# Kernel optimization log

Hardware: AMD Instinct MI355X
Metric: run time of the kernel (lower is better)

## Reference

```python
import jax, jax.numpy as jnp
import numpy as np

LN_EPS = 1e-5

def _conv2d(x, w, b, pad):
    # x: [B,C,H,W], w: [O,I,kh,kw] -> [B,O,H,W]
    y = jax.lax.conv_general_dilated(
        x, w, window_strides=(1, 1), padding=[(pad, pad), (pad, pad)],
        dimension_numbers=('NCHW', 'OIHW', 'NCHW'))
    return y + b[None, :, None, None]

def setup_inputs() -> dict:
    key = jax.random.key(0)
    ks = jax.random.split(key, 12)
    B, C, H, W = 4, 256, 64, 64
    D = 64  # inner_projection
    s_in = 1.0 / np.sqrt(C)
    s_d1 = 1.0 / np.sqrt(D)
    s_d3 = 1.0 / np.sqrt(D * 9)
    return {
        'x':     jax.random.normal(ks[0], (B, C, H, W), jnp.float32),
        'w_in':  jax.random.normal(ks[1], (D, C, 1, 1), jnp.float32) * s_in,
        'b_in':  jnp.zeros((D,), jnp.float32),
        'wq':    jax.random.normal(ks[2], (D, D, 3, 3), jnp.float32) * s_d3,
        'bq':    jnp.zeros((D,), jnp.float32),
        'wk':    jax.random.normal(ks[3], (D, D, 3, 3), jnp.float32) * s_d3,
        'bk':    jnp.zeros((D,), jnp.float32),
        'wv':    jax.random.normal(ks[4], (D, D, 3, 3), jnp.float32) * s_d3,
        'bv':    jnp.zeros((D,), jnp.float32),
        'w_out': jax.random.normal(ks[5], (C, D, 1, 1), jnp.float32) * s_d1,
        'b_out': jnp.zeros((C,), jnp.float32),
        'gamma': jax.random.normal(ks[6], (1,), jnp.float32) * 0.1,
        'ln_w':  jnp.ones((C,), jnp.float32),
        'ln_b':  jnp.zeros((C,), jnp.float32),
    }

def _attention(q, k, v):
    # full-pixel attention, NO 1/sqrt(d) scale (matches source)
    B, C, H, W = v.shape
    N = H * W
    qf = q.reshape(B, -1, N)   # [B,d,N]
    kf = k.reshape(B, -1, N)
    vf = v.reshape(B, -1, N)
    energy = jnp.einsum('bci,bcj->bij', qf, kf)      # [B,N,N] = Q^T K
    attn = jax.nn.softmax(energy, axis=-1)
    out = jnp.einsum('bcj,bij->bci', vf, attn)        # V @ attn^T
    return out.reshape(B, C, H, W)

def _layernorm2d(x, w, b):
    # normalize over channel dim per pixel (LayerNorm2d)
    mu = jnp.mean(x, axis=1, keepdims=True)
    var = jnp.var(x, axis=1, keepdims=True)
    xn = (x - mu) * jax.lax.rsqrt(var + LN_EPS)
    return xn * w[None, :, None, None] + b[None, :, None, None]

def reference(x, w_in, b_in, wq, bq, wk, bk, wv, bv, w_out, b_out, gamma, ln_w, ln_b):
    att = _conv2d(x, w_in, b_in, 0)          # inner projection [B,D,H,W]
    q = _conv2d(att, wq, bq, 1)
    k = _conv2d(att, wk, bk, 1)
    v = _conv2d(att, wv, bv, 1)
    att = _attention(q, k, v)
    att = _conv2d(att, w_out, b_out, 0)       # outer projection [B,C,H,W]
    return _layernorm2d(gamma * x + att, ln_w, ln_b)
```

## Files before the change

kernel.cpp:

```cpp
#include <hip/hip_runtime.h>
#include <hip/hip_bf16.h>

#define BB 4
#define CC 256
#define DD 64
#define HH 64
#define WW 64
#define NN 4096
#define NSPLIT 4
#define VST 68
#define SM_SHIFT2 92.332482616893664f
#define LOG2E 1.4426950408889634f

typedef __hip_bfloat16 bf16;
typedef __attribute__((ext_vector_type(8))) short bf16x8;
typedef __attribute__((ext_vector_type(4))) float f32x4;
typedef __attribute__((ext_vector_type(4))) short s16x4;

#define MFMA16(a, b, c) __builtin_amdgcn_mfma_f32_16x16x32_bf16(a, b, c, 0, 0, 0)

#if __has_builtin(__builtin_amdgcn_mfma_f32_16x16x16bf16_1k)
static __device__ __forceinline__ f32x4 MFMA16K(s16x4 a, s16x4 b, f32x4 c) {
  return __builtin_amdgcn_mfma_f32_16x16x16bf16_1k(a, b, c, 0, 0, 0);
}
#else
static __device__ __forceinline__ f32x4 MFMA16K(s16x4 a, s16x4 b, f32x4 c) {
  f32x4 d;
  asm("v_mfma_f32_16x16x16_bf16 %0, %1, %2, %3"
      : "=&v"(d) : "v"(a), "v"(b), "v"(c));
  return d;
}
#endif

#if __has_builtin(__builtin_amdgcn_exp2f)
#define EXP2F(x) __builtin_amdgcn_exp2f(x)
#else
#define EXP2F(x) exp2f(x)
#endif

static __device__ __forceinline__ float ldin(const void* p, size_t i, bool isb) {
  return isb ? __bfloat162float(((const bf16*)p)[i]) : ((const float*)p)[i];
}
static __device__ __forceinline__ void stout(void* p, size_t i, float v, bool isb) {
  if (isb) ((bf16*)p)[i] = __float2bfloat16(v);
  else     ((float*)p)[i] = v;
}
static __device__ __forceinline__ unsigned pack2(bf16 a, bf16 b) {
  unsigned short ua = *reinterpret_cast<unsigned short*>(&a);
  unsigned short ub = *reinterpret_cast<unsigned short*>(&b);
  return (unsigned)ua | ((unsigned)ub << 16);
}
static __device__ __forceinline__ bool probe_bf16(const unsigned* lnw) {
  return lnw[0] == 0x3F803F80u;
}

__global__ __launch_bounds__(256) void k_wt(
    const void* __restrict__ wq, const void* __restrict__ wk,
    const void* __restrict__ wv, const void* __restrict__ w_in,
    const void* __restrict__ w_out,
    bf16* __restrict__ Wth, bf16* __restrict__ Wtl,
    bf16* __restrict__ Win_h, bf16* __restrict__ Win_l,
    bf16* __restrict__ Wo_h, bf16* __restrict__ Wo_l,
    const unsigned* __restrict__ lnw) {
  const bool isb = probe_bf16(lnw);
  int u = blockIdx.x * 256 + threadIdx.x;
  if (u < 110592) {
    int c3 = u / 36864, rem = u % 36864;
    int tap = rem / 4096, r2 = rem % 4096;
    int oc = r2 >> 6, ic = r2 & 63;
    const void* w = (c3 == 0) ? wq : ((c3 == 1) ? wk : wv);
    float v = ldin(w, (size_t)oc * 576 + ic * 9 + tap, isb);
    bf16 h = __float2bfloat16(v);
    Wth[u] = h;
    Wtl[u] = __float2bfloat16(v - __bfloat162float(h));
  } else if (u < 126976) {
    int v2 = u - 110592;
    float v = ldin(w_in, v2, isb);
    bf16 h = __float2bfloat16(v);
    Win_h[v2] = h;
    Win_l[v2] = __float2bfloat16(v - __bfloat162float(h));
  } else {
    int v2 = u - 126976;
    float v = ldin(w_out, v2, isb);
    bf16 h = __float2bfloat16(v);
    Wo_h[v2] = h;
    Wo_l[v2] = __float2bfloat16(v - __bfloat162float(h));
  }
}

__global__ __launch_bounds__(256) void k_conv_in(
    const void* __restrict__ x,
    const bf16* __restrict__ Win_h, const bf16* __restrict__ Win_l,
    const void* __restrict__ bias, bf16* __restrict__ att_h,
    bf16* __restrict__ att_l, const unsigned* __restrict__ lnw) {
  __shared__ __align__(16) short Xh[32 * 64];
  __shared__ __align__(16) short Xl[32 * 64];
  const bool isb = probe_bf16(lnw);
  const int b = blockIdx.y, n0 = blockIdx.x * 32;
  const int t = threadIdx.x;
  const int w = t >> 6, lane = t & 63, quad = lane >> 4, l16 = lane & 15;
  const int l7 = l16 & 7;
  const size_t xoff = (size_t)b * CC * NN;
  const int sdd = t >> 3, sn4 = (t & 7) * 4;
  f32x4 acc[2];
  #pragma unroll
  for (int nt = 0; nt < 2; ++nt)
    #pragma unroll
    for (int r = 0; r < 4; ++r)
      acc[nt][r] = ldin(bias, w * 16 + quad * 4 + r, isb);
  for (int c0 = 0; c0 < CC; c0 += 64) {
    __syncthreads();
    {
      float a0[4], a1[4];
      size_t i0a = xoff + (size_t)(c0 + 2 * sdd) * NN + n0 + sn4;
      if (!isb) {
        const float* xp = (const float*)x;
        float4 va = *(const float4*)&xp[i0a];
        float4 vb = *(const float4*)&xp[i0a + NN];
        a0[0] = va.x; a0[1] = va.y; a0[2] = va.z; a0[3] = va.w;
        a1[0] = vb.x; a1[1] = vb.y; a1[2] = vb.z; a1[3] = vb.w;
      } else {
        #pragma unroll
        for (int j = 0; j < 4; ++j) {
          a0[j] = ldin(x, i0a + j, true);
          a1[j] = ldin(x, i0a + NN + j, true);
        }
      }
      #pragma unroll
      for (int j = 0; j < 4; ++j) {
        int n = sn4 + j;
        bf16 h0 = __float2bfloat16(a0[j]), h1 = __float2bfloat16(a1[j]);
        bf16 l0 = __float2bfloat16(a0[j] - __bfloat162float(h0));
        bf16 l1 = __float2bfloat16(a1[j] - __bfloat162float(h1));
        int cs = ((sdd >> 2) ^ (n & 7)) * 8 + ((2 * sdd) & 7);
        *(unsigned*)&Xh[n * 64 + cs] = pack2(h0, h1);
        *(unsigned*)&Xl[n * 64 + cs] = pack2(l0, l1);
      }
    }
    __syncthreads();
    #pragma unroll
    for (int kc = 0; kc < 2; ++kc) {
      size_t woff = (size_t)(w * 16 + l16) * 256 + c0 + kc * 32 + quad * 8;
      bf16x8 wh = *(const bf16x8*)(Win_h + woff);
      bf16x8 wl = *(const bf16x8*)(Win_l + woff);
      const int xo = ((kc * 4 + quad) ^ l7) * 8;
      #pragma unroll
      for (int nt = 0; nt < 2; ++nt) {
        int rn = nt * 16 + l16;
        bf16x8 xh = *(const bf16x8*)&Xh[rn * 64 + xo];
        bf16x8 xl = *(const bf16x8*)&Xl[rn * 64 + xo];
        acc[nt] = MFMA16(wh, xh, acc[nt]);
        acc[nt] = MFMA16(wh, xl, acc[nt]);
        acc[nt] = MFMA16(wl, xh, acc[nt]);
      }
    }
  }
  #pragma unroll
  for (int nt = 0; nt < 2; ++nt) {
    size_t off = ((size_t)b * NN + n0 + nt * 16 + l16) * DD + w * 16 + quad * 4;
    bf16 h[4], l[4];
    #pragma unroll
    for (int r = 0; r < 4; ++r) {
      float v = acc[nt][r];
      h[r] = __float2bfloat16(v);
      l[r] = __float2bfloat16(v - __bfloat162float(h[r]));
    }
    *(uint2*)&att_h[off] = make_uint2(pack2(h[0], h[1]), pack2(h[2], h[3]));
    *(uint2*)&att_l[off] = make_uint2(pack2(l[0], l[1]), pack2(l[2], l[3]));
  }
}

__global__ __launch_bounds__(256) void k_conv3(
    const bf16* __restrict__ att_h, const bf16* __restrict__ att_l,
    const bf16* __restrict__ Wth, const bf16* __restrict__ Wtl,
    const void* __restrict__ bq, const void* __restrict__ bk,
    const void* __restrict__ bv,
    bf16* __restrict__ qth, bf16* __restrict__ qtl,
    bf16* __restrict__ kth, bf16* __restrict__ ktl,
    bf16* __restrict__ vt, const unsigned* __restrict__ lnw) {
  __shared__ __align__(16) short Ah[3 * 66 * 64];
  __shared__ __align__(16) short Al[3 * 66 * 64];
  float* o_s = reinterpret_cast<float*>(Ah);
  const bool isb = probe_bf16(lnw);
  const int y = blockIdx.x, b = blockIdx.y, c3 = blockIdx.z;
  const int t = threadIdx.x;
  const int w = t >> 6, lane = t & 63, quad = lane >> 4, l16 = lane & 15;
  const uint4 z4 = make_uint4(0, 0, 0, 0);
  #pragma unroll
  for (int r = 0; r < 3; ++r) {
    int yp = y + r - 1;
    bool ok = (unsigned)yp < 64u;
    const uint4* sh = (const uint4*)(att_h + ((size_t)b * NN + (size_t)yp * 64) * DD);
    const uint4* sl = (const uint4*)(att_l + ((size_t)b * NN + (size_t)yp * 64) * DD);
    #pragma unroll
    for (int ii = 0; ii < 2; ++ii) {
      int u = t + ii * 256;
      int xx = u >> 3, ch = u & 7;
      int rr = r * 66 + xx + 1;
      uint4 vh = ok ? sh[u] : z4;
      uint4 vl = ok ? sl[u] : z4;
      int cs = (ch ^ (rr & 7)) * 8;
      *(uint4*)&Ah[rr * 64 + cs] = vh;
      *(uint4*)&Al[rr * 64 + cs] = vl;
    }
    if (t < 16) {
      int rr = r * 66 + ((t & 1) ? 65 : 0);
      int cs = (t >> 1) * 8;
      *(uint4*)&Ah[rr * 64 + cs] = z4;
      *(uint4*)&Al[rr * 64 + cs] = z4;
    }
  }
  __syncthreads();
  const void* bp = (c3 == 0) ? bq : ((c3 == 1) ? bk : bv);
  const bf16* wth = Wth + (size_t)c3 * 9 * 4096;
  const bf16* wtl = Wtl + (size_t)c3 * 9 * 4096;
  f32x4 acc[4];
  #pragma unroll
  for (int nt = 0; nt < 4; ++nt)
    #pragma unroll
    for (int r = 0; r < 4; ++r)
      acc[nt][r] = ldin(bp, w * 16 + quad * 4 + r, isb);
  #pragma unroll
  for (int tap = 0; tap < 9; ++tap) {
    const int dy = tap / 3, dx = tap % 3;
    const int woff = tap * 4096 + (w * 16 + l16) * 64 + quad * 8;
    bf16x8 wh0 = *(const bf16x8*)(wth + woff);
    bf16x8 wh1 = *(const bf16x8*)(wth + woff + 32);
    bf16x8 wl0 = *(const bf16x8*)(wtl + woff);
    bf16x8 wl1 = *(const bf16x8*)(wtl + woff + 32);
    #pragma unroll
    for (int nt = 0; nt < 4; ++nt) {
      int rr = dy * 66 + nt * 16 + l16 + dx;
      int chA = (quad ^ (rr & 7)) * 8;
      int chB = ((quad + 4) ^ (rr & 7)) * 8;
      bf16x8 ah0 = *(const bf16x8*)&Ah[rr * 64 + chA];
      bf16x8 ah1 = *(const bf16x8*)&Ah[rr * 64 + chB];
      bf16x8 al0 = *(const bf16x8*)&Al[rr * 64 + chA];
      bf16x8 al1 = *(const bf16x8*)&Al[rr * 64 + chB];
      acc[nt] = MFMA16(wh0, ah0, acc[nt]);
      acc[nt] = MFMA16(wh1, ah1, acc[nt]);
      acc[nt] = MFMA16(wh0, al0, acc[nt]);
      acc[nt] = MFMA16(wh1, al1, acc[nt]);
      acc[nt] = MFMA16(wl0, ah0, acc[nt]);
      acc[nt] = MFMA16(wl1, ah1, acc[nt]);
    }
  }
  if (c3 < 2) {
    bf16* dh = (c3 == 0) ? qth : kth;
    bf16* dl = (c3 == 0) ? qtl : ktl;
    const float qsc = (c3 == 0) ? LOG2E : 1.0f;
    const size_t rowb = (size_t)b * NN + (size_t)y * 64;
    #pragma unroll
    for (int nt = 0; nt < 4; ++nt) {
      size_t off = (rowb + nt * 16 + l16) * DD + w * 16 + quad * 4;
      bf16 h[4], l[4];
      #pragma unroll
      for (int r = 0; r < 4; ++r) {
        float v = acc[nt][r] * qsc;
        h[r] = __float2bfloat16(v);
        l[r] = __float2bfloat16(v - __bfloat162float(h[r]));
      }
      *(uint2*)&dh[off] = make_uint2(pack2(h[0], h[1]), pack2(h[2], h[3]));
      *(uint2*)&dl[off] = make_uint2(pack2(l[0], l[1]), pack2(l[2], l[3]));
    }
  } else {
    __syncthreads();
    #pragma unroll
    for (int nt = 0; nt < 4; ++nt)
      #pragma unroll
      for (int r = 0; r < 4; ++r)
        o_s[(nt * 16 + l16) * 65 + w * 16 + quad * 4 + r] = acc[nt][r];
    __syncthreads();
    #pragma unroll
    for (int i = 0; i < 8; ++i) {
      int u = t + i * 256;
      int c = u >> 5, np = (u & 31) * 2;
      float v0 = o_s[np * 65 + c], v1 = o_s[(np + 1) * 65 + c];
      *(unsigned*)&vt[((size_t)b * DD + c) * NN + (size_t)y * 64 + np] =
          pack2(__float2bfloat16(v0), __float2bfloat16(v1));
    }
  }
}

__global__ __launch_bounds__(256) void k_attn(
    const bf16* __restrict__ qth, const bf16* __restrict__ qtl,
    const bf16* __restrict__ kth, const bf16* __restrict__ ktl,
    const bf16* __restrict__ vt, float* __restrict__ po,
    float* __restrict__ pl) {
  __shared__ __align__(16) short Kh[2][64 * 64];
  __shared__ __align__(16) short Kl[2][64 * 64];
  __shared__ __align__(16) short Vs[3][64 * VST];
  const int b = blockIdx.y, i0 = blockIdx.x * 128, sp = blockIdx.z;
  const int jt0 = sp * (64 / NSPLIT), jt1 = jt0 + (64 / NSPLIT);
  const int t = threadIdx.x;
  const int w = t >> 6, lane = t & 63, quad = lane >> 4, l16 = lane & 15;
  const int l7 = l16 & 7;
  const int xA = (quad ^ l7) * 8;
  const int xB = ((quad + 4) ^ l7) * 8;
  const int sr = t >> 2, m4 = t & 3, sg = m4 * 16;
  const int sc0 = ((2 * m4) ^ (sr & 7)) * 8;
  const int sc1 = ((2 * m4 + 1) ^ (sr & 7)) * 8;
  bf16x8 qf_h0[2], qf_h1[2], qf_l0[2], qf_l1[2];
  #pragma unroll
  for (int is = 0; is < 2; ++is) {
    size_t qoff = ((size_t)b * NN + i0 + is * 64 + w * 16 + l16) * DD + quad * 8;
    qf_h0[is] = *(const bf16x8*)(qth + qoff);
    qf_h1[is] = *(const bf16x8*)(qth + qoff + 32);
    qf_l0[is] = *(const bf16x8*)(qtl + qoff);
    qf_l1[is] = *(const bf16x8*)(qtl + qoff + 32);
  }
  const bf16* khg = kth + ((size_t)b * NN + jt0 * 64 + sr) * DD + sg;
  const bf16* klg = ktl + ((size_t)b * NN + jt0 * 64 + sr) * DD + sg;
  const bf16* vg  = vt  + ((size_t)b * DD + sr) * NN + jt0 * 64 + sg;
  uint4 kh0, kh1, kl0, kl1, vx0, vx1;
  const int s0 = jt0 % 3;
  kh0 = ((const uint4*)khg)[0]; kh1 = ((const uint4*)khg)[1];
  kl0 = ((const uint4*)klg)[0]; kl1 = ((const uint4*)klg)[1];
  vx0 = ((const uint4*)vg)[0];  vx1 = ((const uint4*)vg)[1];
  khg += 64 * DD; klg += 64 * DD; vg += 64;
  *(uint4*)&Kh[0][sr * 64 + sc0] = kh0;    *(uint4*)&Kh[0][sr * 64 + sc1] = kh1;
  *(uint4*)&Kl[0][sr * 64 + sc0] = kl0;    *(uint4*)&Kl[0][sr * 64 + sc1] = kl1;
  *(uint4*)&Vs[s0][sr * VST + sc0] = vx0;  *(uint4*)&Vs[s0][sr * VST + sc1] = vx1;
  kh0 = ((const uint4*)khg)[0]; kh1 = ((const uint4*)khg)[1];
  kl0 = ((const uint4*)klg)[0]; kl1 = ((const uint4*)klg)[1];
  vx0 = ((const uint4*)vg)[0];  vx1 = ((const uint4*)vg)[1];
  khg += 64 * DD; klg += 64 * DD; vg += 64;
  __syncthreads();
  s16x4 onesf;
  onesf[0] = onesf[1] = onesf[2] = onesf[3] = (short)0x3F80;
  f32x4 lacc[2] = {};
  f32x4 oacc[4][2] = {};
  s16x4 pfP[2][4];
  int vw = (s0 + 1 == 3) ? 0 : s0 + 1;
  int vr = s0;
  {
    const short* khp = Kh[0];
    const short* klp = Kl[0];
    __builtin_amdgcn_s_setprio(1);
    #pragma unroll
    for (int mt = 0; mt < 4; ++mt) {
      int r0 = (mt * 16 + l16) * 64;
      bf16x8 kf_h0 = *(const bf16x8*)&khp[r0 + xA];
      bf16x8 kf_h1 = *(const bf16x8*)&khp[r0 + xB];
      bf16x8 kf_l0 = *(const bf16x8*)&klp[r0 + xA];
      bf16x8 kf_l1 = *(const bf16x8*)&klp[r0 + xB];
      f32x4 c0 = {0.f, 0.f, 0.f, 0.f}, c1 = {0.f, 0.f, 0.f, 0.f};
      c0 = MFMA16(kf_h0, qf_h0[0], c0);  c0 = MFMA16(kf_h1, qf_h1[0], c0);
      c0 = MFMA16(kf_h0, qf_l0[0], c0);  c0 = MFMA16(kf_h1, qf_l1[0], c0);
      c0 = MFMA16(kf_l0, qf_h0[0], c0);  c0 = MFMA16(kf_l1, qf_h1[0], c0);
      c1 = MFMA16(kf_h0, qf_h0[1], c1);  c1 = MFMA16(kf_h1, qf_h1[1], c1);
      c1 = MFMA16(kf_h0, qf_l0[1], c1);  c1 = MFMA16(kf_h1, qf_l1[1], c1);
      c1 = MFMA16(kf_l0, qf_h0[1], c1);  c1 = MFMA16(kf_l1, qf_h1[1], c1);
      #pragma unroll
      for (int r = 0; r < 4; ++r) {
        float e0 = EXP2F(c0[r] - SM_SHIFT2);
        float e1 = EXP2F(c1[r] - SM_SHIFT2);
        bf16 p0 = __float2bfloat16(e0), p1 = __float2bfloat16(e1);
        pfP[0][mt][r] = *reinterpret_cast<short*>(&p0);
        pfP[1][mt][r] = *reinterpret_cast<short*>(&p1);
      }
    }
    __builtin_amdgcn_s_setprio(0);
    *(uint4*)&Kh[1][sr * 64 + sc0] = kh0;    *(uint4*)&Kh[1][sr * 64 + sc1] = kh1;
    *(uint4*)&Kl[1][sr * 64 + sc0] = kl0;    *(uint4*)&Kl[1][sr * 64 + sc1] = kl1;
    *(uint4*)&Vs[vw][sr * VST + sc0] = vx0;  *(uint4*)&Vs[vw][sr * VST + sc1] = vx1;
    vw = (vw + 1 == 3) ? 0 : vw + 1;
    kh0 = ((const uint4*)khg)[0]; kh1 = ((const uint4*)khg)[1];
    kl0 = ((const uint4*)klg)[0]; kl1 = ((const uint4*)klg)[1];
    vx0 = ((const uint4*)vg)[0];  vx1 = ((const uint4*)vg)[1];
    khg += 64 * DD; klg += 64 * DD; vg += 64;
    __syncthreads();
  }
  for (int jt = jt0 + 1; jt < jt1; ++jt) {
    const short* khp = Kh[jt & 1];
    const short* klp = Kl[jt & 1];
    const short* vpp = Vs[vr];
    s16x4 pfC[2][4];
    __builtin_amdgcn_s_setprio(1);
    #pragma unroll
    for (int mt = 0; mt < 4; ++mt) {
      int r0 = (mt * 16 + l16) * 64;
      bf16x8 kf_h0 = *(const bf16x8*)&khp[r0 + xA];
      bf16x8 kf_h1 = *(const bf16x8*)&khp[r0 + xB];
      bf16x8 kf_l0 = *(const bf16x8*)&klp[r0 + xA];
      bf16x8 kf_l1 = *(const bf16x8*)&klp[r0 + xB];
      f32x4 c0 = {0.f, 0.f, 0.f, 0.f}, c1 = {0.f, 0.f, 0.f, 0.f};
      c0 = MFMA16(kf_h0, qf_h0[0], c0);  c0 = MFMA16(kf_h1, qf_h1[0], c0);
      c0 = MFMA16(kf_h0, qf_l0[0], c0);  c0 = MFMA16(kf_h1, qf_l1[0], c0);
      c0 = MFMA16(kf_l0, qf_h0[0], c0);  c0 = MFMA16(kf_l1, qf_h1[0], c0);
      c1 = MFMA16(kf_h0, qf_h0[1], c1);  c1 = MFMA16(kf_h1, qf_h1[1], c1);
      c1 = MFMA16(kf_h0, qf_l0[1], c1);  c1 = MFMA16(kf_h1, qf_l1[1], c1);
      c1 = MFMA16(kf_l0, qf_h0[1], c1);  c1 = MFMA16(kf_l1, qf_h1[1], c1);
      {
        int rv = (mt * 16 + l16) * VST;
        #pragma unroll
        for (int kt = 0; kt < 4; ++kt) {
          s16x4 vf = *(const s16x4*)
              &vpp[rv + ((kt * 2 + (quad >> 1)) ^ l7) * 8 + (quad & 1) * 4];
          oacc[mt][0] = MFMA16K(vf, pfP[0][kt], oacc[mt][0]);
          oacc[mt][1] = MFMA16K(vf, pfP[1][kt], oacc[mt][1]);
        }
        lacc[0] = MFMA16K(onesf, pfP[0][mt], lacc[0]);
        lacc[1] = MFMA16K(onesf, pfP[1][mt], lacc[1]);
      }
      #pragma unroll
      for (int r = 0; r < 4; ++r) {
        float e0 = EXP2F(c0[r] - SM_SHIFT2);
        float e1 = EXP2F(c1[r] - SM_SHIFT2);
        bf16 p0 = __float2bfloat16(e0), p1 = __float2bfloat16(e1);
        pfC[0][mt][r] = *reinterpret_cast<short*>(&p0);
        pfC[1][mt][r] = *reinterpret_cast<short*>(&p1);
      }
    }
    __builtin_amdgcn_s_setprio(0);
    if (jt + 1 < jt1) {
      short* khn = Kh[(jt + 1) & 1];
      short* kln = Kl[(jt + 1) & 1];
      short* vsn = Vs[vw];
      *(uint4*)&khn[sr * 64 + sc0] = kh0;  *(uint4*)&khn[sr * 64 + sc1] = kh1;
      *(uint4*)&kln[sr * 64 + sc0] = kl0;  *(uint4*)&kln[sr * 64 + sc1] = kl1;
      *(uint4*)&vsn[sr * VST + sc0] = vx0; *(uint4*)&vsn[sr * VST + sc1] = vx1;
    }
    vw = (vw + 1 == 3) ? 0 : vw + 1;
    vr = (vr + 1 == 3) ? 0 : vr + 1;
    if (jt + 2 < jt1) {
      kh0 = ((const uint4*)khg)[0]; kh1 = ((const uint4*)khg)[1];
      kl0 = ((const uint4*)klg)[0]; kl1 = ((const uint4*)klg)[1];
      vx0 = ((const uint4*)vg)[0];  vx1 = ((const uint4*)vg)[1];
      khg += 64 * DD; klg += 64 * DD; vg += 64;
    }
    __syncthreads();
    #pragma unroll
    for (int is = 0; is < 2; ++is)
      #pragma unroll
      for (int m2 = 0; m2 < 4; ++m2) pfP[is][m2] = pfC[is][m2];
  }
  {
    const short* vpp = Vs[vr];
    __builtin_amdgcn_s_setprio(1);
    #pragma unroll
    for (int mt = 0; mt < 4; ++mt) {
      int rv = (mt * 16 + l16) * VST;
      #pragma unroll
      for (int kt = 0; kt < 4; ++kt) {
        s16x4 vf = *(const s16x4*)
            &vpp[rv + ((kt * 2 + (quad >> 1)) ^ l7) * 8 + (quad & 1) * 4];
        oacc[mt][0] = MFMA16K(vf, pfP[0][kt], oacc[mt][0]);
        oacc[mt][1] = MFMA16K(vf, pfP[1][kt], oacc[mt][1]);
      }
      lacc[0] = MFMA16K(onesf, pfP[0][mt], lacc[0]);
      lacc[1] = MFMA16K(onesf, pfP[1][mt], lacc[1]);
    }
    __builtin_amdgcn_s_setprio(0);
  }
  const size_t SEGC = (size_t)BB * DD * NN;
  #pragma unroll
  for (int is = 0; is < 2; ++is) {
    const int ig = i0 + is * 64 + w * 16 + l16;
    #pragma unroll
    for (int mt = 0; mt < 4; ++mt)
      #pragma unroll
      for (int r = 0; r < 4; ++r) {
        int c = mt * 16 + quad * 4 + r;
        po[(size_t)sp * SEGC + ((size_t)b * DD + c) * NN + ig] = oacc[mt][is][r];
      }
    if (quad == 0) pl[((size_t)sp * BB + b) * NN + ig] = lacc[is][0];
  }
}

__global__ __launch_bounds__(256) void k_out_ln(
    const float* __restrict__ po, const float* __restrict__ pl,
    const void* __restrict__ x,
    const bf16* __restrict__ Wo_h, const bf16* __restrict__ Wo_l,
    const void* __restrict__ bias, const void* __restrict__ gamma,
    const void* __restrict__ lw, const void* __restrict__ lb,
    void* __restrict__ out, const unsigned* __restrict__ lnw) {
  __shared__ __align__(16) short Ahs[32 * 64];
  __shared__ __align__(16) short Als[32 * 64];
  __shared__ __align__(16) float Obuf[256 * 36];
  __shared__ float inv_s[32];
  __shared__ float red1[32 * 4], red2[32 * 4];
  __shared__ float mu_s[32], rs_s[32];
  __shared__ float lw_s[256], lb_s[256];
  const bool isb = probe_bf16(lnw);
  const int b = blockIdx.y, n0 = blockIdx.x * 32;
  const int t = threadIdx.x;
  const int w = t >> 6, lane = t & 63, quad = lane >> 4, l16 = lane & 15;
  const int l7 = l16 & 7;
  const size_t SEGC = (size_t)BB * DD * NN;
  if (t < 32) {
    int i = n0 + t;
    float lsum = 0.f;
    #pragma unroll
    for (int s = 0; s < NSPLIT; ++s) lsum += pl[((size_t)s * BB + b) * NN + i];
    inv_s[t] = 1.f / lsum;
  }
  lw_s[t] = ldin(lw, t, isb);
  lb_s[t] = ldin(lb, t, isb);
  const float g = ldin(gamma, 0, isb);
  __syncthreads();
  {
    const int dd = t >> 3, n4 = (t & 7) * 4;
    size_t base = ((size_t)b * DD + 2 * dd) * NN + n0 + n4;
    float v0[4] = {0.f, 0.f, 0.f, 0.f}, v1[4] = {0.f, 0.f, 0.f, 0.f};
    #pragma unroll
    for (int s = 0; s < NSPLIT; ++s) {
      float4 pa = *(const float4*)&po[(size_t)s * SEGC + base];
      float4 pb = *(const float4*)&po[(size_t)s * SEGC + base + NN];
      v0[0] += pa.x; v0[1] += pa.y; v0[2] += pa.z; v0[3] += pa.w;
      v1[0] += pb.x; v1[1] += pb.y; v1[2] += pb.z; v1[3] += pb.w;
    }
    #pragma unroll
    for (int j = 0; j < 4; ++j) {
      int n = n4 + j;
      float inv = inv_s[n];
      float a0 = v0[j] * inv, a1 = v1[j] * inv;
      bf16 h0 = __float2bfloat16(a0), h1 = __float2bfloat16(a1);
      bf16 l0 = __float2bfloat16(a0 - __bfloat162float(h0));
      bf16 l1 = __float2bfloat16(a1 - __bfloat162float(h1));
      int cs = ((dd >> 2) ^ (n & 7)) * 8 + ((2 * dd) & 7);
      *(unsigned*)&Ahs[n * 64 + cs] = pack2(h0, h1);
      *(unsigned*)&Als[n * 64 + cs] = pack2(l0, l1);
    }
  }
  f32x4 acc[4][2];
  #pragma unroll
  for (int oct = 0; oct < 4; ++oct)
    #pragma unroll
    for (int r = 0; r < 4; ++r) {
      float bo = ldin(bias, w * 64 + oct * 16 + quad * 4 + r, isb);
      #pragma unroll
      for (int nt = 0; nt < 2; ++nt) acc[oct][nt][r] = bo;
    }
  __syncthreads();
  #pragma unroll
  for (int oct = 0; oct < 4; ++oct) {
    const int base = w * 64 + oct * 16;
    #pragma unroll
    for (int kc = 0; kc < 2; ++kc) {
      size_t woff = (size_t)(base + l16) * 64 + kc * 32 + quad * 8;
      bf16x8 wh = *(const bf16x8*)(Wo_h + woff);
      bf16x8 wl = *(const bf16x8*)(Wo_l + woff);
      const int xo = ((kc * 4 + quad) ^ l7) * 8;
      #pragma unroll
      for (int nt = 0; nt < 2; ++nt) {
        int rn = nt * 16 + l16;
        bf16x8 ah = *(const bf16x8*)&Ahs[rn * 64 + xo];
        bf16x8 al = *(const bf16x8*)&Als[rn * 64 + xo];
        acc[oct][nt] = MFMA16(wh, ah, acc[oct][nt]);
        acc[oct][nt] = MFMA16(wh, al, acc[oct][nt]);
        acc[oct][nt] = MFMA16(wl, ah, acc[oct][nt]);
      }
    }
  }
  #pragma unroll
  for (int nt = 0; nt < 2; ++nt) {
    int nn = nt * 16 + l16;
    float s1 = 0.f, s2 = 0.f;
    #pragma unroll
    for (int oct = 0; oct < 4; ++oct)
      #pragma unroll
      for (int r = 0; r < 4; ++r) {
        int oc = w * 64 + oct * 16 + quad * 4 + r;
        float xv = ldin(x, ((size_t)b * CC + oc) * NN + n0 + nn, isb);
        float y = acc[oct][nt][r] + g * xv;
        acc[oct][nt][r] = y;
        s1 += y; s2 += y * y;
      }
    s1 += __shfl_xor(s1, 16, 64); s1 += __shfl_xor(s1, 32, 64);
    s2 += __shfl_xor(s2, 16, 64); s2 += __shfl_xor(s2, 32, 64);
    if (quad == 0) { red1[nn * 4 + w] = s1; red2[nn * 4 + w] = s2; }
  }
  __syncthreads();
  if (t < 32) {
    float sm = red1[t * 4] + red1[t * 4 + 1] + red1[t * 4 + 2] + red1[t * 4 + 3];
    float sq = red2[t * 4] + red2[t * 4 + 1] + red2[t * 4 + 2] + red2[t * 4 + 3];
    float mu = sm * (1.f / 256.f);
    float var = sq * (1.f / 256.f) - mu * mu;
    mu_s[t] = mu;
    rs_s[t] = rsqrtf(var + 1e-5f);
  }
  __syncthreads();
  if (!isb) {
    #pragma unroll
    for (int nt = 0; nt < 2; ++nt) {
      int nn = nt * 16 + l16;
      float mu = mu_s[nn], rs = rs_s[nn];
      #pragma unroll
      for (int oct = 0; oct < 4; ++oct)
        #pragma unroll
        for (int r = 0; r < 4; ++r) {
          int oc = w * 64 + oct * 16 + quad * 4 + r;
          Obuf[oc * 36 + nn] = (acc[oct][nt][r] - mu) * rs * lw_s[oc] + lb_s[oc];
        }
    }
    __syncthreads();
    const int oc8 = t >> 3, pxq = (t & 7) * 4;
    float* op = (float*)out + (size_t)b * CC * NN + n0 + pxq;
    #pragma unroll
    for (int p2 = 0; p2 < 8; ++p2) {
      int oc = p2 * 32 + oc8;
      float4 v = *(const float4*)&Obuf[oc * 36 + pxq];
      *(float4*)&op[(size_t)oc * NN] = v;
    }
  } else {
    #pragma unroll
    for (int nt = 0; nt < 2; ++nt) {
      int nn = nt * 16 + l16;
      float mu = mu_s[nn], rs = rs_s[nn];
      #pragma unroll
      for (int oct = 0; oct < 4; ++oct)
        #pragma unroll
        for (int r = 0; r < 4; ++r) {
          int oc = w * 64 + oct * 16 + quad * 4 + r;
          float o = (acc[oct][nt][r] - mu) * rs * lw_s[oc] + lb_s[oc];
          stout(out, ((size_t)b * CC + oc) * NN + n0 + nn, o, isb);
        }
    }
  }
}

extern "C" void kernel_launch(void* const* d_in, const int* in_sizes, int n_in,
                              void* d_out, int out_size, void* d_ws, size_t ws_size,
                              hipStream_t stream) {
  const void* x     = d_in[0];
  const void* w_in  = d_in[1];
  const void* b_in  = d_in[2];
  const void* wq    = d_in[3];
  const void* bq    = d_in[4];
  const void* wk    = d_in[5];
  const void* bk    = d_in[6];
  const void* wv    = d_in[7];
  const void* bv    = d_in[8];
  const void* w_out = d_in[9];
  const void* b_out = d_in[10];
  const void* gamma = d_in[11];
  const void* ln_w  = d_in[12];
  const void* ln_b  = d_in[13];

  const size_t SEG = (size_t)BB * DD * NN;
  char*  p     = (char*)d_ws;
  bf16*  att_h = (bf16*)p;  p += SEG * 2;
  bf16*  att_l = (bf16*)p;  p += SEG * 2;
  bf16*  qth   = (bf16*)p;  p += SEG * 2;
  bf16*  qtl   = (bf16*)p;  p += SEG * 2;
  bf16*  kth   = (bf16*)p;  p += SEG * 2;
  bf16*  ktl   = (bf16*)p;  p += SEG * 2;
  bf16*  vt    = (bf16*)p;  p += SEG * 2;
  float* po    = (float*)p; p += (size_t)NSPLIT * SEG * 4;
  float* pl    = (float*)p; p += (size_t)NSPLIT * BB * NN * 4;
  bf16*  Wth   = (bf16*)p;  p += 110592 * 2;
  bf16*  Wtl   = (bf16*)p;  p += 110592 * 2;
  bf16*  Win_h = (bf16*)p;  p += 16384 * 2;
  bf16*  Win_l = (bf16*)p;  p += 16384 * 2;
  bf16*  Wo_h  = (bf16*)p;  p += 16384 * 2;
  bf16*  Wo_l  = (bf16*)p;  p += 16384 * 2;
  const unsigned* lnw = (const unsigned*)ln_w;

  k_wt<<<560, 256, 0, stream>>>(wq, wk, wv, w_in, w_out, Wth, Wtl,
                                Win_h, Win_l, Wo_h, Wo_l, lnw);
  k_conv_in<<<dim3(NN / 32, BB), 256, 0, stream>>>(x, Win_h, Win_l, b_in,
                                                   att_h, att_l, lnw);
  k_conv3<<<dim3(64, BB, 3), 256, 0, stream>>>(att_h, att_l, Wth, Wtl,
                                               bq, bk, bv,
                                               qth, qtl, kth, ktl, vt, lnw);
  k_attn<<<dim3(NN / 128, BB, NSPLIT), 256, 0, stream>>>(qth, qtl, kth, ktl, vt,
                                                         po, pl);
  k_out_ln<<<dim3(NN / 32, BB), 256, 0, stream>>>(po, pl, x, Wo_h, Wo_l,
                                                  b_out, gamma, ln_w, ln_b,
                                                  d_out, lnw);
}
```

Measured before the change: 172.8 us.

## Unroll attention pipeline by two with ping-pong registers and remap block IDs

The attention main loop becomes a macro body unrolled in pairs, with pfA and pfB swapping roles. This removes the per-iteration register copy of probabilities and the modulo buffer index arithmetic, and precomputes V swizzle offsets. Block indices are also remapped so that the eight consecutive launch IDs spread across splits, batches and query tiles, which changes cache and XCD locality. The loop trip count is hardcoded to the NSPLIT=4 tile count (16 iterations), so changing NSPLIT would break it.

```diff
diff --git a/kernel.cpp b/kernel.cpp
--- a/kernel.cpp
+++ b/kernel.cpp
@@ -282,6 +282,59 @@
   }
 }
 
+#define ATTN_BODY(PFIN, PFOUT, KRDH, KRDL, KSTH, KSTL, DOSTAGE, DOPREF)       \
+  {                                                                           \
+    __builtin_amdgcn_s_setprio(1);                                            \
+    _Pragma("unroll")                                                         \
+    for (int mt = 0; mt < 4; ++mt) {                                          \
+      int r0 = (mt * 16 + l16) * 64;                                          \
+      bf16x8 kf_h0 = *(const bf16x8*)&KRDH[r0 + xA];                          \
+      bf16x8 kf_h1 = *(const bf16x8*)&KRDH[r0 + xB];                          \
+      bf16x8 kf_l0 = *(const bf16x8*)&KRDL[r0 + xA];                          \
+      bf16x8 kf_l1 = *(const bf16x8*)&KRDL[r0 + xB];                          \
+      f32x4 c0 = {0.f, 0.f, 0.f, 0.f}, c1 = {0.f, 0.f, 0.f, 0.f};             \
+      c0 = MFMA16(kf_h0, qf_h0[0], c0);  c0 = MFMA16(kf_h1, qf_h1[0], c0);    \
+      c0 = MFMA16(kf_h0, qf_l0[0], c0);  c0 = MFMA16(kf_h1, qf_l1[0], c0);    \
+      c0 = MFMA16(kf_l0, qf_h0[0], c0);  c0 = MFMA16(kf_l1, qf_h1[0], c0);    \
+      c1 = MFMA16(kf_h0, qf_h0[1], c1);  c1 = MFMA16(kf_h1, qf_h1[1], c1);    \
+      c1 = MFMA16(kf_h0, qf_l0[1], c1);  c1 = MFMA16(kf_h1, qf_l1[1], c1);    \
+      c1 = MFMA16(kf_l0, qf_h0[1], c1);  c1 = MFMA16(kf_l1, qf_h1[1], c1);    \
+      {                                                                       \
+        int rv = (mt * 16 + l16) * VST;                                       \
+        _Pragma("unroll")                                                     \
+        for (int kt = 0; kt < 4; ++kt) {                                      \
+          s16x4 vf = *(const s16x4*)&vR[rv + vofs[kt]];                       \
+          oacc[mt][0] = MFMA16K(vf, PFIN[0][kt], oacc[mt][0]);                \
+          oacc[mt][1] = MFMA16K(vf, PFIN[1][kt], oacc[mt][1]);                \
+        }                                                                     \
+        lacc[0] = MFMA16K(onesf, PFIN[0][mt], lacc[0]);                       \
+        lacc[1] = MFMA16K(onesf, PFIN[1][mt], lacc[1]);                       \
+      }                                                                       \
+      _Pragma("unroll")                                                       \
+      for (int r = 0; r < 4; ++r) {                                           \
+        float e0 = EXP2F(c0[r] - SM_SHIFT2);                                  \
+        float e1 = EXP2F(c1[r] - SM_SHIFT2);                                  \
+        bf16 p0 = __float2bfloat16(e0), p1 = __float2bfloat16(e1);            \
+        PFOUT[0][mt][r] = *reinterpret_cast<short*>(&p0);                     \
+        PFOUT[1][mt][r] = *reinterpret_cast<short*>(&p1);                     \
+      }                                                                       \
+    }                                                                         \
+    __builtin_amdgcn_s_setprio(0);                                            \
+    if (DOSTAGE) {                                                            \
+      *(uint4*)&KSTH[sk0] = kh0;  *(uint4*)&KSTH[sk1] = kh1;                  \
+      *(uint4*)&KSTL[sk0] = kl0;  *(uint4*)&KSTL[sk1] = kl1;                  \
+      *(uint4*)&vW[sv0] = vx0;    *(uint4*)&vW[sv1] = vx1;                    \
+    }                                                                         \
+    if (DOPREF) {                                                             \
+      kh0 = ((const uint4*)khg)[0]; kh1 = ((const uint4*)khg)[1];             \
+      kl0 = ((const uint4*)klg)[0]; kl1 = ((const uint4*)klg)[1];             \
+      vx0 = ((const uint4*)vg)[0];  vx1 = ((const uint4*)vg)[1];              \
+      khg += 64 * DD; klg += 64 * DD; vg += 64;                               \
+    }                                                                         \
+    __syncthreads();                                                          \
+    { short* rt_ = vR; vR = vM; vM = vW; vW = rt_; }                          \
+  }
+
 __global__ __launch_bounds__(256) void k_attn(
     const bf16* __restrict__ qth, const bf16* __restrict__ qtl,
     const bf16* __restrict__ kth, const bf16* __restrict__ ktl,
@@ -290,7 +343,9 @@
   __shared__ __align__(16) short Kh[2][64 * 64];
   __shared__ __align__(16) short Kl[2][64 * 64];
   __shared__ __align__(16) short Vs[3][64 * VST];
-  const int b = blockIdx.y, i0 = blockIdx.x * 128, sp = blockIdx.z;
+  const int lid = blockIdx.x + 32 * blockIdx.y + 128 * blockIdx.z;
+  const int myid = (lid & 7) * 64 + (lid >> 3);
+  const int b = (myid >> 5) & 3, i0 = (myid & 31) * 128, sp = myid >> 7;
   const int jt0 = sp * (64 / NSPLIT), jt1 = jt0 + (64 / NSPLIT);
   const int t = threadIdx.x;
   const int w = t >> 6, lane = t & 63, quad = lane >> 4, l16 = lane & 15;
@@ -298,8 +353,14 @@
   const int xA = (quad ^ l7) * 8;
   const int xB = ((quad + 4) ^ l7) * 8;
   const int sr = t >> 2, m4 = t & 3, sg = m4 * 16;
-  const int sc0 = ((2 * m4) ^ (sr & 7)) * 8;
-  const int sc1 = ((2 * m4 + 1) ^ (sr & 7)) * 8;
+  const int sk0 = sr * 64 + ((2 * m4) ^ (sr & 7)) * 8;
+  const int sk1 = sr * 64 + ((2 * m4 + 1) ^ (sr & 7)) * 8;
+  const int sv0 = sr * VST + ((2 * m4) ^ (sr & 7)) * 8;
+  const int sv1 = sr * VST + ((2 * m4 + 1) ^ (sr & 7)) * 8;
+  int vofs[4];
+  #pragma unroll
+  for (int kt = 0; kt < 4; ++kt)
+    vofs[kt] = ((kt * 2 + (quad >> 1)) ^ l7) * 8 + (quad & 1) * 4;
   bf16x8 qf_h0[2], qf_h1[2], qf_l0[2], qf_l1[2];
   #pragma unroll
   for (int is = 0; is < 2; ++is) {
@@ -314,13 +375,16 @@
   const bf16* vg  = vt  + ((size_t)b * DD + sr) * NN + jt0 * 64 + sg;
   uint4 kh0, kh1, kl0, kl1, vx0, vx1;
   const int s0 = jt0 % 3;
+  short* vR = Vs[s0];
+  short* vM = Vs[(s0 + 1 == 3) ? 0 : s0 + 1];
+  short* vW = Vs[(s0 + 2 >= 3) ? s0 + 2 - 3 : s0 + 2];
   kh0 = ((const uint4*)khg)[0]; kh1 = ((const uint4*)khg)[1];
   kl0 = ((const uint4*)klg)[0]; kl1 = ((const uint4*)klg)[1];
   vx0 = ((const uint4*)vg)[0];  vx1 = ((const uint4*)vg)[1];
   khg += 64 * DD; klg += 64 * DD; vg += 64;
-  *(uint4*)&Kh[0][sr * 64 + sc0] = kh0;    *(uint4*)&Kh[0][sr * 64 + sc1] = kh1;
-  *(uint4*)&Kl[0][sr * 64 + sc0] = kl0;    *(uint4*)&Kl[0][sr * 64 + sc1] = kl1;
-  *(uint4*)&Vs[s0][sr * VST + sc0] = vx0;  *(uint4*)&Vs[s0][sr * VST + sc1] = vx1;
+  *(uint4*)&Kh[0][sk0] = kh0;  *(uint4*)&Kh[0][sk1] = kh1;
+  *(uint4*)&Kl[0][sk0] = kl0;  *(uint4*)&Kl[0][sk1] = kl1;
+  *(uint4*)&vR[sv0] = vx0;     *(uint4*)&vR[sv1] = vx1;
   kh0 = ((const uint4*)khg)[0]; kh1 = ((const uint4*)khg)[1];
   kl0 = ((const uint4*)klg)[0]; kl1 = ((const uint4*)klg)[1];
   vx0 = ((const uint4*)vg)[0];  vx1 = ((const uint4*)vg)[1];
@@ -330,20 +394,18 @@
   onesf[0] = onesf[1] = onesf[2] = onesf[3] = (short)0x3F80;
   f32x4 lacc[2] = {};
   f32x4 oacc[4][2] = {};
-  s16x4 pfP[2][4];
-  int vw = (s0 + 1 == 3) ? 0 : s0 + 1;
-  int vr = s0;
+  s16x4 pfA[2][4], pfB[2][4];
+  short* const kh0p = Kh[0];  short* const kh1p = Kh[1];
+  short* const kl0p = Kl[0];  short* const kl1p = Kl[1];
   {
-    const short* khp = Kh[0];
-    const short* klp = Kl[0];
     __builtin_amdgcn_s_setprio(1);
     #pragma unroll
     for (int mt = 0; mt < 4; ++mt) {
       int r0 = (mt * 16 + l16) * 64;
-      bf16x8 kf_h0 = *(const bf16x8*)&khp[r0 + xA];
-      bf16x8 kf_h1 = *(const bf16x8*)&khp[r0 + xB];
-      bf16x8 kf_l0 = *(const bf16x8*)&klp[r0 + xA];
-      bf16x8 kf_l1 = *(const bf16x8*)&klp[r0 + xB];
+      bf16x8 kf_h0 = *(const bf16x8*)&kh0p[r0 + xA];
+      bf16x8 kf_h1 = *(const bf16x8*)&kh0p[r0 + xB];
+      bf16x8 kf_l0 = *(const bf16x8*)&kl0p[r0 + xA];
+      bf16x8 kf_l1 = *(const bf16x8*)&kl0p[r0 + xB];
       f32x4 c0 = {0.f, 0.f, 0.f, 0.f}, c1 = {0.f, 0.f, 0.f, 0.f};
       c0 = MFMA16(kf_h0, qf_h0[0], c0);  c0 = MFMA16(kf_h1, qf_h1[0], c0);
       c0 = MFMA16(kf_h0, qf_l0[0], c0);  c0 = MFMA16(kf_h1, qf_l1[0], c0);
@@ -356,100 +418,40 @@
         float e0 = EXP2F(c0[r] - SM_SHIFT2);
         float e1 = EXP2F(c1[r] - SM_SHIFT2);
         bf16 p0 = __float2bfloat16(e0), p1 = __float2bfloat16(e1);
-        pfP[0][mt][r] = *reinterpret_cast<short*>(&p0);
-        pfP[1][mt][r] = *reinterpret_cast<short*>(&p1);
+        pfA[0][mt][r] = *reinterpret_cast<short*>(&p0);
+        pfA[1][mt][r] = *reinterpret_cast<short*>(&p1);
       }
     }
     __builtin_amdgcn_s_setprio(0);
-    *(uint4*)&Kh[1][sr * 64 + sc0] = kh0;    *(uint4*)&Kh[1][sr * 64 + sc1] = kh1;
-    *(uint4*)&Kl[1][sr * 64 + sc0] = kl0;    *(uint4*)&Kl[1][sr * 64 + sc1] = kl1;
-    *(uint4*)&Vs[vw][sr * VST + sc0] = vx0;  *(uint4*)&Vs[vw][sr * VST + sc1] = vx1;
-    vw = (vw + 1 == 3) ? 0 : vw + 1;
+    *(uint4*)&kh1p[sk0] = kh0;  *(uint4*)&kh1p[sk1] = kh1;
+    *(uint4*)&kl1p[sk0] = kl0;  *(uint4*)&kl1p[sk1] = kl1;
+    *(uint4*)&vM[sv0] = vx0;    *(uint4*)&vM[sv1] = vx1;
     kh0 = ((const uint4*)khg)[0]; kh1 = ((const uint4*)khg)[1];
     kl0 = ((const uint4*)klg)[0]; kl1 = ((const uint4*)klg)[1];
     vx0 = ((const uint4*)vg)[0];  vx1 = ((const uint4*)vg)[1];
     khg += 64 * DD; klg += 64 * DD; vg += 64;
     __syncthreads();
   }
-  for (int jt = jt0 + 1; jt < jt1; ++jt) {
-    const short* khp = Kh[jt & 1];
-    const short* klp = Kl[jt & 1];
-    const short* vpp = Vs[vr];
-    s16x4 pfC[2][4];
-    __builtin_amdgcn_s_setprio(1);
-    #pragma unroll
-    for (int mt = 0; mt < 4; ++mt) {
-      int r0 = (mt * 16 + l16) * 64;
-      bf16x8 kf_h0 = *(const bf16x8*)&khp[r0 + xA];
-      bf16x8 kf_h1 = *(const bf16x8*)&khp[r0 + xB];
-      bf16x8 kf_l0 = *(const bf16x8*)&klp[r0 + xA];
-      bf16x8 kf_l1 = *(const bf16x8*)&klp[r0 + xB];
-      f32x4 c0 = {0.f, 0.f, 0.f, 0.f}, c1 = {0.f, 0.f, 0.f, 0.f};
-      c0 = MFMA16(kf_h0, qf_h0[0], c0);  c0 = MFMA16(kf_h1, qf_h1[0], c0);
-      c0 = MFMA16(kf_h0, qf_l0[0], c0);  c0 = MFMA16(kf_h1, qf_l1[0], c0);
-      c0 = MFMA16(kf_l0, qf_h0[0], c0);  c0 = MFMA16(kf_l1, qf_h1[0], c0);
-      c1 = MFMA16(kf_h0, qf_h0[1], c1);  c1 = MFMA16(kf_h1, qf_h1[1], c1);
-      c1 = MFMA16(kf_h0, qf_l0[1], c1);  c1 = MFMA16(kf_h1, qf_l1[1], c1);
-      c1 = MFMA16(kf_l0, qf_h0[1], c1);  c1 = MFMA16(kf_l1, qf_h1[1], c1);
-      {
-        int rv = (mt * 16 + l16) * VST;
-        #pragma unroll
-        for (int kt = 0; kt < 4; ++kt) {
-          s16x4 vf = *(const s16x4*)
-              &vpp[rv + ((kt * 2 + (quad >> 1)) ^ l7) * 8 + (quad & 1) * 4];
-          oacc[mt][0] = MFMA16K(vf, pfP[0][kt], oacc[mt][0]);
-          oacc[mt][1] = MFMA16K(vf, pfP[1][kt], oacc[mt][1]);
-        }
-        lacc[0] = MFMA16K(onesf, pfP[0][mt], lacc[0]);
-        lacc[1] = MFMA16K(onesf, pfP[1][mt], lacc[1]);
-      }
-      #pragma unroll
-      for (int r = 0; r < 4; ++r) {
-        float e0 = EXP2F(c0[r] - SM_SHIFT2);
-        float e1 = EXP2F(c1[r] - SM_SHIFT2);
-        bf16 p0 = __float2bfloat16(e0), p1 = __float2bfloat16(e1);
-        pfC[0][mt][r] = *reinterpret_cast<short*>(&p0);
-        pfC[1][mt][r] = *reinterpret_cast<short*>(&p1);
-      }
-    }
-    __builtin_amdgcn_s_setprio(0);
-    if (jt + 1 < jt1) {
-      short* khn = Kh[(jt + 1) & 1];
-      short* kln = Kl[(jt + 1) & 1];
-      short* vsn = Vs[vw];
-      *(uint4*)&khn[sr * 64 + sc0] = kh0;  *(uint4*)&khn[sr * 64 + sc1] = kh1;
-      *(uint4*)&kln[sr * 64 + sc0] = kl0;  *(uint4*)&kln[sr * 64 + sc1] = kl1;
-      *(uint4*)&vsn[sr * VST + sc0] = vx0; *(uint4*)&vsn[sr * VST + sc1] = vx1;
-    }
-    vw = (vw + 1 == 3) ? 0 : vw + 1;
-    vr = (vr + 1 == 3) ? 0 : vr + 1;
-    if (jt + 2 < jt1) {
-      kh0 = ((const uint4*)khg)[0]; kh1 = ((const uint4*)khg)[1];
-      kl0 = ((const uint4*)klg)[0]; kl1 = ((const uint4*)klg)[1];
-      vx0 = ((const uint4*)vg)[0];  vx1 = ((const uint4*)vg)[1];
-      khg += 64 * DD; klg += 64 * DD; vg += 64;
-    }
-    __syncthreads();
-    #pragma unroll
-    for (int is = 0; is < 2; ++is)
-      #pragma unroll
-      for (int m2 = 0; m2 < 4; ++m2) pfP[is][m2] = pfC[is][m2];
-  }
+  for (int m = 0; m < 6; ++m) {
+    ATTN_BODY(pfA, pfB, kh1p, kl1p, kh0p, kl0p, true, true)
+    ATTN_BODY(pfB, pfA, kh0p, kl0p, kh1p, kl1p, true, true)
+  }
+  ATTN_BODY(pfA, pfB, kh1p, kl1p, kh0p, kl0p, true, true)
+  ATTN_BODY(pfB, pfA, kh0p, kl0p, kh1p, kl1p, true, false)
+  ATTN_BODY(pfA, pfB, kh1p, kl1p, kh0p, kl0p, false, false)
   {
-    const short* vpp = Vs[vr];
     __builtin_amdgcn_s_setprio(1);
     #pragma unroll
     for (int mt = 0; mt < 4; ++mt) {
       int rv = (mt * 16 + l16) * VST;
       #pragma unroll
       for (int kt = 0; kt < 4; ++kt) {
-        s16x4 vf = *(const s16x4*)
-            &vpp[rv + ((kt * 2 + (quad >> 1)) ^ l7) * 8 + (quad & 1) * 4];
-        oacc[mt][0] = MFMA16K(vf, pfP[0][kt], oacc[mt][0]);
-        oacc[mt][1] = MFMA16K(vf, pfP[1][kt], oacc[mt][1]);
-      }
-      lacc[0] = MFMA16K(onesf, pfP[0][mt], lacc[0]);
-      lacc[1] = MFMA16K(onesf, pfP[1][mt], lacc[1]);
+        s16x4 vf = *(const s16x4*)&vR[rv + vofs[kt]];
+        oacc[mt][0] = MFMA16K(vf, pfB[0][kt], oacc[mt][0]);
+        oacc[mt][1] = MFMA16K(vf, pfB[1][kt], oacc[mt][1]);
+      }
+      lacc[0] = MFMA16K(onesf, pfB[0][mt], lacc[0]);
+      lacc[1] = MFMA16K(onesf, pfB[1][mt], lacc[1]);
     }
     __builtin_amdgcn_s_setprio(0);
   }
```

After: 184.4 us. 6.7% more time.
